# Optimization experiments

Hardware: AMD Instinct MI355X
Metric: run time of the kernel (lower is better)

## Reference

```python
import jax, jax.numpy as jnp
import numpy as np

B = 32          # batch_size (scenes)
P_PER_B = 256   # proposals per scene (max_n_proposals, equal by construction)
N = B * P_PER_B # total proposals = 8192
PTS = 1024      # points per proposal
M = 128         # cfg.m, instance feature dim
LANG = 256      # lang_size
H = 128         # hidden_size
EPS = 1e-5      # BatchNorm eps


def setup_inputs() -> dict:
    key = jax.random.key(0)
    ks = jax.random.split(key, 16)
    feats = jax.random.normal(ks[0], (N, M), jnp.float32)
    total_pts = N * PTS
    # proposals_idx: (total_pts, 2) = [proposal_id, global_point_id]; points are
    # contiguous per proposal, proposals contiguous per scene.
    prop_ids = jnp.repeat(jnp.arange(N, dtype=jnp.int32), PTS)
    pt_ids = jnp.arange(total_pts, dtype=jnp.int32)
    proposals_idx = jnp.stack([prop_ids, pt_ids], axis=1)
    proposals_offset = jnp.arange(N + 1, dtype=jnp.int32) * PTS
    b_offsets = jnp.arange(B + 1, dtype=jnp.int32) * (P_PER_B * PTS)
    lang_emb = jax.random.normal(ks[1], (B, LANG), jnp.float32)
    # parameters: fuse = Conv1d(LANG+M -> H, k=1) + ReLU
    W_fuse = jax.random.normal(ks[2], (H, LANG + M), jnp.float32) * 0.05
    b_fuse = jnp.zeros((H,), jnp.float32)
    # match = Conv1d(H,H,1)+ReLU+BN, Conv1d(H,H,1)+ReLU+BN, Conv1d(H,1,1)
    W1 = jax.random.normal(ks[3], (H, H), jnp.float32) * 0.05
    b1 = jnp.zeros((H,), jnp.float32)
    g1 = jnp.ones((H,), jnp.float32)
    be1 = jnp.zeros((H,), jnp.float32)
    rm1 = jax.random.normal(ks[4], (H,), jnp.float32) * 0.1
    rv1 = jax.random.uniform(ks[5], (H,), jnp.float32, 0.5, 1.5)
    W2 = jax.random.normal(ks[6], (H, H), jnp.float32) * 0.05
    b2 = jnp.zeros((H,), jnp.float32)
    g2 = jnp.ones((H,), jnp.float32)
    be2 = jnp.zeros((H,), jnp.float32)
    rm2 = jax.random.normal(ks[7], (H,), jnp.float32) * 0.1
    rv2 = jax.random.uniform(ks[8], (H,), jnp.float32, 0.5, 1.5)
    W3 = jax.random.normal(ks[9], (1, H), jnp.float32) * 0.05
    b3 = jnp.zeros((1,), jnp.float32)
    return {
        'aggregated_vote_features': feats,
        'proposals_idx': proposals_idx,
        'proposals_offset': proposals_offset,
        'b_offsets': b_offsets,
        'lang_emb': lang_emb,
        'W_fuse': W_fuse, 'b_fuse': b_fuse,
        'W1': W1, 'b1': b1, 'g1': g1, 'be1': be1, 'rm1': rm1, 'rv1': rv1,
        'W2': W2, 'b2': b2, 'g2': g2, 'be2': be2, 'rm2': rm2, 'rv2': rv2,
        'W3': W3, 'b3': b3,
    }


def _bn(x, g, be, rm, rv):
    # eval-mode BatchNorm1d over channel dim of (B, C, P)
    scale = g / jnp.sqrt(rv + EPS)
    return (x - rm[None, :, None]) * scale[None, :, None] + be[None, :, None]


def reference(aggregated_vote_features, proposals_idx, proposals_offset, b_offsets,
              lang_emb, W_fuse, b_fuse, W1, b1, g1, be1, rm1, rv1,
              W2, b2, g2, be2, rm2, rv2, W3, b3):
    # --- vectorized replacement of the host-sync batch-id loop ---
    first_pts = proposals_idx[proposals_offset[:-1], 1]            # (N,) first point of each proposal
    bid = jnp.searchsorted(b_offsets, first_pts, side='right') - 1  # (N,) proposal_batch_ids
    # --- ragged -> padded gather (vectorized scatter by per-batch position) ---
    counts = jax.ops.segment_sum(jnp.ones_like(bid), bid, num_segments=B)
    offs = jnp.concatenate([jnp.zeros((1,), counts.dtype), jnp.cumsum(counts)[:-1]])
    order = jnp.argsort(bid)                                       # stable sort keeps original order per batch
    bid_s = bid[order]
    pos = jnp.arange(bid.shape[0]) - offs[bid_s]                   # position within its batch
    padded = jnp.zeros((B, P_PER_B, M), aggregated_vote_features.dtype)
    padded = padded.at[bid_s, pos].set(aggregated_vote_features[order])  # (B, P, M)
    # --- concat language features and run 1x1 conv chain ---
    lang = jnp.broadcast_to(lang_emb[:, None, :], (B, P_PER_B, LANG))
    x = jnp.concatenate([padded, lang], axis=-1)                   # (B, P, M+LANG)
    x = jnp.einsum('bpc,oc->bop', x, W_fuse) + b_fuse[None, :, None]
    x = jax.nn.relu(x)                                             # fuse
    x = _bn(jax.nn.relu(jnp.einsum('bcp,oc->bop', x, W1) + b1[None, :, None]), g1, be1, rm1, rv1)
    x = _bn(jax.nn.relu(jnp.einsum('bcp,oc->bop', x, W2) + b2[None, :, None]), g2, be2, rm2, rv2)
    conf = jnp.einsum('bcp,oc->bop', x, W3) + b3[None, :, None]    # (B, 1, P)
    return conf[:, 0, :]                                           # cluster_ref: (B, P)
```

## Files before the change

### kernel.cpp

```cpp
#include <hip/hip_runtime.h>
#include <math.h>

#define B_    32
#define PPB   256
#define N_    (B_*PPB)
#define M_    128
#define LANG_ 256
#define H_    128
#define EPS_  1e-5f
#define MC    16
#define WA_OFF 120832

typedef __attribute__((ext_vector_type(8))) short s16x8;
typedef __attribute__((ext_vector_type(4))) float f32x4;

static __device__ __forceinline__ unsigned short f2bf(float x) {
  unsigned int u = __float_as_uint(x);
  unsigned int r = (u + 0x7fff + ((u >> 16) & 1)) >> 16;
  return (unsigned short)r;
}
static __device__ __forceinline__ float bf2f(unsigned short h) {
  return __uint_as_float(((unsigned int)h) << 16);
}

__global__ __launch_bounds__(256) void k_map_a(
    const int* __restrict__ pidx, const int* __restrict__ poff,
    const int* __restrict__ boff, int* __restrict__ bid_g,
    int* __restrict__ wrank_g, int* __restrict__ hist_g,
    int* __restrict__ src_of_dest,
    const float* __restrict__ Wf, const float* __restrict__ lang,
    float* __restrict__ lp,
    const float* __restrict__ W1, const float* __restrict__ W2,
    unsigned short* __restrict__ wa)
{
  __shared__ int sb[33];
  __shared__ int wh[4][32];
  const int tid = threadIdx.x;
  const int i = blockIdx.x * 256 + tid;
  const int lane = tid & 63, wid = tid >> 6;
  if (tid < 33) sb[tid] = boff[tid];
  __syncthreads();
  const int off = poff[i];
  const int fp  = pidx[2 * off + 1];
  int cnt = 0;
  #pragma unroll
  for (int j = 0; j < 33; ++j) cnt += (sb[j] <= fp) ? 1 : 0;
  int bd = cnt - 1;
  bd = bd < 0 ? 0 : (bd > 31 ? 31 : bd);
  bid_g[i] = bd;
  src_of_dest[i] = -1;

  unsigned long long mym = 0;
  #pragma unroll
  for (int k = 0; k < 32; ++k) {
    const unsigned long long m = __ballot(bd == k);
    if (bd == k) mym = m;
    if (lane == k) wh[wid][k] = __popcll(m);
  }
  const int rw = __popcll(mym & ((1ull << lane) - 1ull));
  __syncthreads();
  int base = 0;
  #pragma unroll
  for (int w = 0; w < 4; ++w) if (w < wid) base += wh[w][bd];
  wrank_g[i] = base + rw;
  if (tid < 32) hist_g[blockIdx.x * 32 + tid] =
      wh[0][tid] + wh[1][tid] + wh[2][tid] + wh[3][tid];

  {
    const int o = tid >> 1, hf = tid & 1;
    float acc = 0.f;
    const int l0 = hf * 128;
    #pragma unroll 8
    for (int l = l0; l < l0 + 128; l += 4) {
      const float4 w = *reinterpret_cast<const float4*>(Wf + o * 384 + 128 + l);
      const float4 e = *reinterpret_cast<const float4*>(lang + blockIdx.x * LANG_ + l);
      acc += w.x * e.x + w.y * e.y + w.z * e.z + w.w * e.w;
    }
    acc += __shfl_xor(acc, 1);
    if (hf == 0) lp[blockIdx.x * H_ + o] = acc;
  }

  for (int G = blockIdx.x * 4 + wid; G < 192; G += 128) {
    const int L = G >> 6, s = (G >> 3) & 7, t = G & 7;
    const float* Wsrc; int str;
    if (L == 0)      { Wsrc = Wf; str = 384; }
    else if (L == 1) { Wsrc = W1; str = H_; }
    else             { Wsrc = W2; str = H_; }
    const int o = t * 16 + (lane & 15), g = lane >> 4, sp = s & 3;
    const bool hi = (s < 4);
    const float* rowp = Wsrc + (size_t)o * str + sp * 32 + g * 4;
    const float4 a = *reinterpret_cast<const float4*>(rowp);
    const float4 bq = *reinterpret_cast<const float4*>(rowp + 16);
    const float av[8] = {a.x, a.y, a.z, a.w, bq.x, bq.y, bq.z, bq.w};
    s16x8 v;
    #pragma unroll
    for (int e = 0; e < 8; ++e) {
      const unsigned short h = f2bf(av[e]);
      v[e] = (short)(hi ? h : f2bf(av[e] - bf2f(h)));
    }
    *reinterpret_cast<s16x8*>(wa + (size_t)G * 512 + lane * 8) = v;
  }
}

__global__ __launch_bounds__(256) void k_scat(
    const int* __restrict__ bid_g, const int* __restrict__ wrank_g,
    const int* __restrict__ hist_g, int* __restrict__ src_of_dest)
{
  __shared__ int sh[8][32];
  __shared__ int cb[32];
  const int c = blockIdx.x, tid = threadIdx.x;
  const int u = tid >> 5, bin = tid & 31;
  int run = 0;
  #pragma unroll
  for (int p = 0; p < 4; ++p) {
    const int cc = u + 8 * p;
    if (cc < c) run += hist_g[cc * 32 + bin];
  }
  sh[u][bin] = run;
  __syncthreads();
  if (tid < 32) {
    int s = 0;
    #pragma unroll
    for (int w = 0; w < 8; ++w) s += sh[w][tid];
    cb[tid] = s;
  }
  __syncthreads();
  const int i = c * 256 + tid;
  const int bd = bid_g[i];
  const int rank = cb[bd] + wrank_g[i];
  if (rank < PPB) src_of_dest[bd * PPB + rank] = i;
}

#define MFMA_LAYER(Aarr)                                                     \
  {                                                                          \
    _Pragma("unroll")                                                        \
    for (int sg = 0; sg < 8; ++sg) {                                         \
      const s16x8 bb = (sg < 4) ? Bh[sg] : Bl[sg - 4];                       \
      acc[0] = __builtin_amdgcn_mfma_f32_16x16x32_bf16(Aarr[0][sg], bb, acc[0], 0, 0, 0); \
      acc[1] = __builtin_amdgcn_mfma_f32_16x16x32_bf16(Aarr[1][sg], bb, acc[1], 0, 0, 0); \
    }                                                                        \
    _Pragma("unroll")                                                        \
    for (int sg = 0; sg < 8; ++sg) {                                         \
      const s16x8 bb = (sg < 4) ? Bl[sg] : Bh[sg - 4];                       \
      acc[0] = __builtin_amdgcn_mfma_f32_16x16x32_bf16(Aarr[0][sg], bb, acc[0], 0, 0, 0); \
      acc[1] = __builtin_amdgcn_mfma_f32_16x16x32_bf16(Aarr[1][sg], bb, acc[1], 0, 0, 0); \
    }                                                                        \
  }

#define READ_B()                                                             \
  {                                                                          \
    _Pragma("unroll")                                                        \
    for (int s = 0; s < 4; ++s) {                                            \
      const int idx = (s * 4 + g) * 16 + o16;                                \
      Bh[s] = XbHi[idx];                                                     \
      Bl[s] = XbLo[idx];                                                     \
    }                                                                        \
  }

#define LOAD_A(Aarr, LL)                                                     \
  {                                                                          \
    _Pragma("unroll")                                                        \
    for (int t = 0; t < 2; ++t)                                              \
      _Pragma("unroll")                                                      \
      for (int s = 0; s < 8; ++s)                                            \
        Aarr[t][s] = *reinterpret_cast<const s16x8*>(                        \
            wa + (size_t)(((LL) * 8 + s) * 8 + (wid * 2 + t)) * 512 + lane * 8); \
  }

__global__ __launch_bounds__(256, 2) void k_mlp(
    const float* __restrict__ feats,
    const unsigned short* __restrict__ wa,
    const float* __restrict__ bf, const float* __restrict__ b1,
    const float* __restrict__ g1, const float* __restrict__ be1,
    const float* __restrict__ rm1, const float* __restrict__ rv1,
    const float* __restrict__ b2, const float* __restrict__ g2,
    const float* __restrict__ be2, const float* __restrict__ rm2,
    const float* __restrict__ rv2,
    const float* __restrict__ W3, const float* __restrict__ b3,
    const int* __restrict__ srcmap, const float* __restrict__ lpg,
    float* __restrict__ out)
{
  __shared__ s16x8 XbHi[256];
  __shared__ s16x8 XbLo[256];
  __shared__ float pbuf[1024];
  __shared__ float outp[64];

  const int tid = threadIdx.x;
  const int lane = tid & 63, wid = tid >> 6;
  const int o16 = lane & 15, g = lane >> 4;
  const int q0 = blockIdx.x * MC;
  const int b = blockIdx.x >> 4;

  s16x8 A0[2][8], A1[2][8], A2[2][8];
  LOAD_A(A0, 0);

  #pragma unroll
  for (int j = tid; j < 1024; j += 256) {
    const int arr = j >> 7, o = j & 127;
    float v;
    switch (arr) {
      case 0: v = bf[o] + lpg[b * H_ + o]; break;
      case 1: v = b1[o]; break;
      case 2: v = g1[o] * rsqrtf(rv1[o] + EPS_); break;
      case 3: { const float s = g1[o] * rsqrtf(rv1[o] + EPS_);
                v = be1[o] - rm1[o] * s; } break;
      case 4: v = b2[o]; break;
      case 5: v = g2[o] * rsqrtf(rv2[o] + EPS_); break;
      case 6: { const float s = g2[o] * rsqrtf(rv2[o] + EPS_);
                v = be2[o] - rm2[o] * s; } break;
      default: v = W3[o]; break;
    }
    pbuf[j] = v;
  }

  {
    const int n = tid & 15, u = tid >> 4;
    const int s = u >> 2, gg = u & 3;
    const int srow = srcmap[q0 + n];
    const int k0 = s * 32 + gg * 4;
    float4 a = make_float4(0.f, 0.f, 0.f, 0.f), bq = a;
    if (srow >= 0) {
      a  = *reinterpret_cast<const float4*>(feats + (size_t)srow * M_ + k0);
      bq = *reinterpret_cast<const float4*>(feats + (size_t)srow * M_ + k0 + 16);
    }
    const float av[8] = {a.x, a.y, a.z, a.w, bq.x, bq.y, bq.z, bq.w};
    s16x8 hv, lv;
    #pragma unroll
    for (int e = 0; e < 8; ++e) {
      const unsigned short h = f2bf(av[e]);
      hv[e] = (short)h;
      lv[e] = (short)f2bf(av[e] - bf2f(h));
    }
    XbHi[u * 16 + n] = hv;
    XbLo[u * 16 + n] = lv;
  }
  __syncthreads();

  f32x4 acc[2];
  s16x8 Bh[4], Bl[4];

  READ_B();
  __syncthreads();
  LOAD_A(A1, 1);
  acc[0] = (f32x4){0.f, 0.f, 0.f, 0.f};
  acc[1] = (f32x4){0.f, 0.f, 0.f, 0.f};
  MFMA_LAYER(A0);
  {
    s16x8 hv, lv;
    #pragma unroll
    for (int t = 0; t < 2; ++t)
      #pragma unroll
      for (int r = 0; r < 4; ++r) {
        const int o = (wid * 2 + t) * 16 + g * 4 + r;
        const float v = fmaxf(acc[t][r] + pbuf[o], 0.f);
        const unsigned short h = f2bf(v);
        hv[t * 4 + r] = (short)h;
        lv[t * 4 + r] = (short)f2bf(v - bf2f(h));
      }
    const int widx = (wid * 4 + g) * 16 + o16;
    XbHi[widx] = hv;
    XbLo[widx] = lv;
  }
  __syncthreads();

  READ_B();
  __syncthreads();
  LOAD_A(A2, 2);
  acc[0] = (f32x4){0.f, 0.f, 0.f, 0.f};
  acc[1] = (f32x4){0.f, 0.f, 0.f, 0.f};
  MFMA_LAYER(A1);
  {
    s16x8 hv, lv;
    #pragma unroll
    for (int t = 0; t < 2; ++t)
      #pragma unroll
      for (int r = 0; r < 4; ++r) {
        const int o = (wid * 2 + t) * 16 + g * 4 + r;
        const float v = fmaxf(acc[t][r] + pbuf[128 + o], 0.f) * pbuf[256 + o]
                        + pbuf[384 + o];
        const unsigned short h = f2bf(v);
        hv[t * 4 + r] = (short)h;
        lv[t * 4 + r] = (short)f2bf(v - bf2f(h));
      }
    const int widx = (wid * 4 + g) * 16 + o16;
    XbHi[widx] = hv;
    XbLo[widx] = lv;
  }
  __syncthreads();

  READ_B();
  acc[0] = (f32x4){0.f, 0.f, 0.f, 0.f};
  acc[1] = (f32x4){0.f, 0.f, 0.f, 0.f};
  MFMA_LAYER(A2);
  {
    float p0 = 0.f;
    #pragma unroll
    for (int t = 0; t < 2; ++t)
      #pragma unroll
      for (int r = 0; r < 4; ++r) {
        const int o = (wid * 2 + t) * 16 + g * 4 + r;
        p0 += pbuf[896 + o] *
              (fmaxf(acc[t][r] + pbuf[512 + o], 0.f) * pbuf[640 + o] + pbuf[768 + o]);
      }
    p0 += __shfl_xor(p0, 16);
    p0 += __shfl_xor(p0, 32);
    if (lane < 16) outp[wid * 16 + lane] = p0;
    __syncthreads();
    if (tid < 16)
      out[q0 + tid] = outp[tid] + outp[16 + tid] + outp[32 + tid] + outp[48 + tid] + b3[0];
  }
}

extern "C" void kernel_launch(void* const* d_in, const int* in_sizes, int n_in,
                              void* d_out, int out_size, void* d_ws, size_t ws_size,
                              hipStream_t stream) {
  const float* feats = (const float*)d_in[0];
  const int*   pidx  = (const int*)d_in[1];
  const int*   poff  = (const int*)d_in[2];
  const int*   boff  = (const int*)d_in[3];
  const float* lang  = (const float*)d_in[4];
  const float* Wf    = (const float*)d_in[5];
  const float* bf    = (const float*)d_in[6];
  const float* W1    = (const float*)d_in[7];
  const float* b1    = (const float*)d_in[8];
  const float* g1    = (const float*)d_in[9];
  const float* be1   = (const float*)d_in[10];
  const float* rm1   = (const float*)d_in[11];
  const float* rv1   = (const float*)d_in[12];
  const float* W2    = (const float*)d_in[13];
  const float* b2    = (const float*)d_in[14];
  const float* g2    = (const float*)d_in[15];
  const float* be2   = (const float*)d_in[16];
  const float* rm2   = (const float*)d_in[17];
  const float* rv2   = (const float*)d_in[18];
  const float* W3    = (const float*)d_in[19];
  const float* b3    = (const float*)d_in[20];
  float* out = (float*)d_out;

  int* srcmap = (int*)d_ws;
  int* bidp   = srcmap + N_;
  int* wrank  = bidp + N_;
  int* hist   = wrank + N_;
  float* lp = (float*)(hist + 32 * 32);
  unsigned short* wa = (unsigned short*)((char*)d_ws + WA_OFF);

  hipLaunchKernelGGL(k_map_a, dim3(32), dim3(256), 0, stream,
                     pidx, poff, boff, bidp, wrank, hist, srcmap,
                     Wf, lang, lp, W1, W2, wa);
  hipLaunchKernelGGL(k_scat, dim3(32), dim3(256), 0, stream,
                     bidp, wrank, hist, srcmap);
  hipLaunchKernelGGL(k_mlp, dim3(N_ / MC), dim3(256), 0, stream,
                     feats, wa, bf, b1, g1, be1, rm1, rv1,
                     b2, g2, be2, rm2, rv2, W3, b3, srcmap, lp, out);
}
```

Measured before the change: 24.34 us.

## Fuse setup and MLP kernels into one cooperative kernel with grid sync

Merges the three launches (batch-id mapping, scatter, MLP) into one cooperative kernel. Setup work (srcmap construction, weight conversion to split bf16, language projection) is spread across the first 96 blocks, followed by a grid-wide barrier before the MLP phase. The srcmap build is rewritten as a per-batch mask scan with prefix sums, replacing the global histogram and scatter pass. This removes two launch gaps and inter-kernel dependencies, but adds a grid.sync across 512 blocks and requires every block to be co-resident.

New measurement: 97.09 us. 299% more time.

```diff
diff --git a/kernel.cpp b/kernel.cpp
--- a/kernel.cpp
+++ b/kernel.cpp
@@ -1,5 +1,8 @@
 #include <hip/hip_runtime.h>
+#include <hip/hip_cooperative_groups.h>
 #include <math.h>
+
+namespace cg = cooperative_groups;
 
 #define B_    32
 #define PPB   256
@@ -9,7 +12,7 @@
 #define H_    128
 #define EPS_  1e-5f
 #define MC    16
-#define WA_OFF 120832
+#define NBLK  (N_/MC)
 
 typedef __attribute__((ext_vector_type(8))) short s16x8;
 typedef __attribute__((ext_vector_type(4))) float f32x4;
@@ -21,114 +24,6 @@
 }
 static __device__ __forceinline__ float bf2f(unsigned short h) {
   return __uint_as_float(((unsigned int)h) << 16);
-}
-
-__global__ __launch_bounds__(256) void k_map_a(
-    const int* __restrict__ pidx, const int* __restrict__ poff,
-    const int* __restrict__ boff, int* __restrict__ bid_g,
-    int* __restrict__ wrank_g, int* __restrict__ hist_g,
-    int* __restrict__ src_of_dest,
-    const float* __restrict__ Wf, const float* __restrict__ lang,
-    float* __restrict__ lp,
-    const float* __restrict__ W1, const float* __restrict__ W2,
-    unsigned short* __restrict__ wa)
-{
-  __shared__ int sb[33];
-  __shared__ int wh[4][32];
-  const int tid = threadIdx.x;
-  const int i = blockIdx.x * 256 + tid;
-  const int lane = tid & 63, wid = tid >> 6;
-  if (tid < 33) sb[tid] = boff[tid];
-  __syncthreads();
-  const int off = poff[i];
-  const int fp  = pidx[2 * off + 1];
-  int cnt = 0;
-  #pragma unroll
-  for (int j = 0; j < 33; ++j) cnt += (sb[j] <= fp) ? 1 : 0;
-  int bd = cnt - 1;
-  bd = bd < 0 ? 0 : (bd > 31 ? 31 : bd);
-  bid_g[i] = bd;
-  src_of_dest[i] = -1;
-
-  unsigned long long mym = 0;
-  #pragma unroll
-  for (int k = 0; k < 32; ++k) {
-    const unsigned long long m = __ballot(bd == k);
-    if (bd == k) mym = m;
-    if (lane == k) wh[wid][k] = __popcll(m);
-  }
-  const int rw = __popcll(mym & ((1ull << lane) - 1ull));
-  __syncthreads();
-  int base = 0;
-  #pragma unroll
-  for (int w = 0; w < 4; ++w) if (w < wid) base += wh[w][bd];
-  wrank_g[i] = base + rw;
-  if (tid < 32) hist_g[blockIdx.x * 32 + tid] =
-      wh[0][tid] + wh[1][tid] + wh[2][tid] + wh[3][tid];
-
-  {
-    const int o = tid >> 1, hf = tid & 1;
-    float acc = 0.f;
-    const int l0 = hf * 128;
-    #pragma unroll 8
-    for (int l = l0; l < l0 + 128; l += 4) {
-      const float4 w = *reinterpret_cast<const float4*>(Wf + o * 384 + 128 + l);
-      const float4 e = *reinterpret_cast<const float4*>(lang + blockIdx.x * LANG_ + l);
-      acc += w.x * e.x + w.y * e.y + w.z * e.z + w.w * e.w;
-    }
-    acc += __shfl_xor(acc, 1);
-    if (hf == 0) lp[blockIdx.x * H_ + o] = acc;
-  }
-
-  for (int G = blockIdx.x * 4 + wid; G < 192; G += 128) {
-    const int L = G >> 6, s = (G >> 3) & 7, t = G & 7;
-    const float* Wsrc; int str;
-    if (L == 0)      { Wsrc = Wf; str = 384; }
-    else if (L == 1) { Wsrc = W1; str = H_; }
-    else             { Wsrc = W2; str = H_; }
-    const int o = t * 16 + (lane & 15), g = lane >> 4, sp = s & 3;
-    const bool hi = (s < 4);
-    const float* rowp = Wsrc + (size_t)o * str + sp * 32 + g * 4;
-    const float4 a = *reinterpret_cast<const float4*>(rowp);
-    const float4 bq = *reinterpret_cast<const float4*>(rowp + 16);
-    const float av[8] = {a.x, a.y, a.z, a.w, bq.x, bq.y, bq.z, bq.w};
-    s16x8 v;
-    #pragma unroll
-    for (int e = 0; e < 8; ++e) {
-      const unsigned short h = f2bf(av[e]);
-      v[e] = (short)(hi ? h : f2bf(av[e] - bf2f(h)));
-    }
-    *reinterpret_cast<s16x8*>(wa + (size_t)G * 512 + lane * 8) = v;
-  }
-}
-
-__global__ __launch_bounds__(256) void k_scat(
-    const int* __restrict__ bid_g, const int* __restrict__ wrank_g,
-    const int* __restrict__ hist_g, int* __restrict__ src_of_dest)
-{
-  __shared__ int sh[8][32];
-  __shared__ int cb[32];
-  const int c = blockIdx.x, tid = threadIdx.x;
-  const int u = tid >> 5, bin = tid & 31;
-  int run = 0;
-  #pragma unroll
-  for (int p = 0; p < 4; ++p) {
-    const int cc = u + 8 * p;
-    if (cc < c) run += hist_g[cc * 32 + bin];
-  }
-  sh[u][bin] = run;
-  __syncthreads();
-  if (tid < 32) {
-    int s = 0;
-    #pragma unroll
-    for (int w = 0; w < 8; ++w) s += sh[w][tid];
-    cb[tid] = s;
-  }
-  __syncthreads();
-  const int i = c * 256 + tid;
-  const int bd = bid_g[i];
-  const int rank = cb[bd] + wrank_g[i];
-  if (rank < PPB) src_of_dest[bd * PPB + rank] = i;
 }
 
 #define MFMA_LAYER(Aarr)                                                     \
@@ -167,39 +62,40 @@
             wa + (size_t)(((LL) * 8 + s) * 8 + (wid * 2 + t)) * 512 + lane * 8); \
   }
 
-__global__ __launch_bounds__(256, 2) void k_mlp(
+__global__ __launch_bounds__(256, 2) void k_all(
     const float* __restrict__ feats,
-    const unsigned short* __restrict__ wa,
-    const float* __restrict__ bf, const float* __restrict__ b1,
+    const int* __restrict__ pidx, const int* __restrict__ poff,
+    const int* __restrict__ boff, const float* __restrict__ langg,
+    const float* __restrict__ Wf, const float* __restrict__ bf,
+    const float* __restrict__ W1, const float* __restrict__ b1,
     const float* __restrict__ g1, const float* __restrict__ be1,
     const float* __restrict__ rm1, const float* __restrict__ rv1,
-    const float* __restrict__ b2, const float* __restrict__ g2,
-    const float* __restrict__ be2, const float* __restrict__ rm2,
-    const float* __restrict__ rv2,
+    const float* __restrict__ W2, const float* __restrict__ b2,
+    const float* __restrict__ g2, const float* __restrict__ be2,
+    const float* __restrict__ rm2, const float* __restrict__ rv2,
     const float* __restrict__ W3, const float* __restrict__ b3,
-    const int* __restrict__ srcmap, const float* __restrict__ lpg,
+    int* __restrict__ srcmap, float* __restrict__ lp,
+    unsigned short* __restrict__ wa,
     float* __restrict__ out)
 {
   __shared__ s16x8 XbHi[256];
   __shared__ s16x8 XbLo[256];
   __shared__ float pbuf[1024];
   __shared__ float outp[64];
+  __shared__ int   wtot[4];
+
+  cg::grid_group grid = cg::this_grid();
 
   const int tid = threadIdx.x;
   const int lane = tid & 63, wid = tid >> 6;
   const int o16 = lane & 15, g = lane >> 4;
-  const int q0 = blockIdx.x * MC;
-  const int b = blockIdx.x >> 4;
-
-  s16x8 A0[2][8], A1[2][8], A2[2][8];
-  LOAD_A(A0, 0);
+  const int blk = blockIdx.x;
 
   #pragma unroll
-  for (int j = tid; j < 1024; j += 256) {
+  for (int j = 128 + tid; j < 1024; j += 256) {
     const int arr = j >> 7, o = j & 127;
     float v;
     switch (arr) {
-      case 0: v = bf[o] + lpg[b * H_ + o]; break;
       case 1: v = b1[o]; break;
       case 2: v = g1[o] * rsqrtf(rv1[o] + EPS_); break;
       case 3: { const float s = g1[o] * rsqrtf(rv1[o] + EPS_);
@@ -212,6 +108,84 @@
     }
     pbuf[j] = v;
   }
+
+  if (blk < 32) {
+    const int blo = boff[blk], bhi = boff[blk + 1];
+    srcmap[blk * PPB + tid] = -1;
+    const int i0 = tid * 32;
+    unsigned mask = 0u;
+    #pragma unroll
+    for (int j = 0; j < 32; ++j) {
+      const int off = poff[i0 + j];
+      const int fp  = pidx[2 * off + 1];
+      mask |= (fp >= blo && fp < bhi) ? (1u << j) : 0u;
+    }
+    const int cnt = __popc(mask);
+    int sc = cnt;
+    #pragma unroll
+    for (int d = 1; d < 64; d <<= 1) {
+      const int v = __shfl_up(sc, d);
+      if (lane >= d) sc += v;
+    }
+    if (lane == 63) wtot[wid] = sc;
+    __syncthreads();
+    int base = sc - cnt;
+    #pragma unroll
+    for (int w = 0; w < 4; ++w) if (w < wid) base += wtot[w];
+    unsigned m = mask;
+    int r = base;
+    while (m) {
+      const int j = __ffs(m) - 1;
+      if (r < PPB) srcmap[blk * PPB + r] = i0 + j;
+      ++r;
+      m &= m - 1;
+    }
+  } else if (blk < 64) {
+    for (int sub = wid; sub < 6; sub += 4) {
+      const int G = (blk - 32) * 6 + sub;
+      const int L = G >> 6, s = (G >> 3) & 7, t = G & 7;
+      const float* Wsrc; int str;
+      if (L == 0)      { Wsrc = Wf; str = 384; }
+      else if (L == 1) { Wsrc = W1; str = H_; }
+      else             { Wsrc = W2; str = H_; }
+      const int o = t * 16 + o16, sp = s & 3;
+      const bool hi = (s < 4);
+      const float* rowp = Wsrc + (size_t)o * str + sp * 32 + g * 4;
+      const float4 a = *reinterpret_cast<const float4*>(rowp);
+      const float4 bq = *reinterpret_cast<const float4*>(rowp + 16);
+      const float av[8] = {a.x, a.y, a.z, a.w, bq.x, bq.y, bq.z, bq.w};
+      s16x8 v;
+      #pragma unroll
+      for (int e = 0; e < 8; ++e) {
+        const unsigned short h = f2bf(av[e]);
+        v[e] = (short)(hi ? h : f2bf(av[e] - bf2f(h)));
+      }
+      *reinterpret_cast<s16x8*>(wa + (size_t)G * 512 + lane * 8) = v;
+    }
+  } else if (blk < 96) {
+    const int bb = blk - 64;
+    const int o = tid >> 1, hf = tid & 1;
+    float acc = 0.f;
+    const int l0 = hf * 128;
+    #pragma unroll 8
+    for (int l = l0; l < l0 + 128; l += 4) {
+      const float4 w = *reinterpret_cast<const float4*>(Wf + o * 384 + 128 + l);
+      const float4 e = *reinterpret_cast<const float4*>(langg + bb * LANG_ + l);
+      acc += w.x * e.x + w.y * e.y + w.z * e.z + w.w * e.w;
+    }
+    acc += __shfl_xor(acc, 1);
+    if (hf == 0) lp[bb * H_ + o] = acc;
+  }
+
+  grid.sync();
+
+  const int q0 = blk * MC;
+  const int b = blk >> 4;
+
+  s16x8 A0[2][8], A1[2][8], A2[2][8];
+  LOAD_A(A0, 0);
+
+  if (tid < 128) pbuf[tid] = bf[tid] + lp[b * H_ + tid];
 
   {
     const int n = tid & 15, u = tid >> 4;
@@ -337,19 +311,19 @@
   const float* b3    = (const float*)d_in[20];
   float* out = (float*)d_out;
 
-  int* srcmap = (int*)d_ws;
-  int* bidp   = srcmap + N_;
-  int* wrank  = bidp + N_;
-  int* hist   = wrank + N_;
-  float* lp = (float*)(hist + 32 * 32);
-  unsigned short* wa = (unsigned short*)((char*)d_ws + WA_OFF);
-
-  hipLaunchKernelGGL(k_map_a, dim3(32), dim3(256), 0, stream,
-                     pidx, poff, boff, bidp, wrank, hist, srcmap,
-                     Wf, lang, lp, W1, W2, wa);
-  hipLaunchKernelGGL(k_scat, dim3(32), dim3(256), 0, stream,
-                     bidp, wrank, hist, srcmap);
-  hipLaunchKernelGGL(k_mlp, dim3(N_ / MC), dim3(256), 0, stream,
-                     feats, wa, bf, b1, g1, be1, rm1, rv1,
-                     b2, g2, be2, rm2, rv2, W3, b3, srcmap, lp, out);
+  int*            srcmap = (int*)d_ws;
+  float*          lp     = (float*)((char*)d_ws + 32768);
+  unsigned short* wa     = (unsigned short*)((char*)d_ws + 49152);
+
+  void* args[] = { (void*)&feats, (void*)&pidx, (void*)&poff, (void*)&boff,
+                   (void*)&lang, (void*)&Wf, (void*)&bf,
+                   (void*)&W1, (void*)&b1, (void*)&g1, (void*)&be1,
+                   (void*)&rm1, (void*)&rv1,
+                   (void*)&W2, (void*)&b2, (void*)&g2, (void*)&be2,
+                   (void*)&rm2, (void*)&rv2,
+                   (void*)&W3, (void*)&b3,
+                   (void*)&srcmap, (void*)&lp, (void*)&wa, (void*)&out };
+
+  hipLaunchCooperativeKernel((void*)k_all, dim3(NBLK), dim3(256),
+                             args, 0, stream);
 }
```
